# Optimization experiments

Measured on AMD Instinct MI355X. Metric: run time of the kernel, lower is better.

The kernel has to match this reference:

```python
import jax, jax.numpy as jnp
import numpy as np

G = 128          # voxel grid extent per axis
B = G + 2        # key base, allows coords in [-1, G] after +1 shift
N_PTS = 100000
C_IN = 32
C_OUT = 32


def _key(c):
    # c: [..., 3] int32 voxel coords in [-1, G]; unique linear key per voxel
    return ((c[..., 0] + 1) * B + (c[..., 1] + 1)) * B + (c[..., 2] + 1)


def setup_inputs() -> dict:
    key = jax.random.key(0)
    k1, k2, k3 = jax.random.split(key, 3)
    positions = jax.random.randint(k1, (N_PTS, 3), 0, G, dtype=jnp.int32)
    features = jax.random.normal(k2, (N_PTS, C_IN), dtype=jnp.float32)
    # per-offset filter matrices, [K^3, Cin, Cout], fan-in style init
    weight = jax.random.normal(k3, (27, C_IN, C_OUT), dtype=jnp.float32) * (1.0 / np.sqrt(27 * C_IN))
    return {"features": features, "positions": positions, "weight": weight}


def reference(features, positions, weight):
    # Submanifold sparse conv: output at the same sparse positions as input.
    # For each of the 27 kernel offsets, hash-lookup the neighbor voxel,
    # gather its feature (or 0 if absent), matmul with the per-offset filter,
    # accumulate. use_bias=False, normalize=False, voxel_size=1.0, offset=0.
    n = features.shape[0]
    keys = _key(positions)                      # [N]
    order = jnp.argsort(keys)
    sk = keys[order]                            # sorted keys (hash table)

    ax = jnp.arange(-1, 2, dtype=jnp.int32)
    off = jnp.stack(jnp.meshgrid(ax, ax, ax, indexing="ij"), axis=-1).reshape(27, 3)

    qk = _key(positions[None, :, :] + off[:, None, :])          # [27, N]
    pos_idx = jnp.clip(jnp.searchsorted(sk, qk), 0, n - 1)      # [27, N]
    match = sk[pos_idx] == qk                                   # neighbor exists?
    gidx = order[pos_idx]                                       # original index of neighbor

    gf = jnp.where(match[..., None], features[gidx], 0.0)       # [27, N, Cin] gather
    out = jnp.einsum("onc,ocd->nd", gf, weight)                 # scatter-accumulate via reduce over o
    return out
```

## Files before the change

kernel.cpp:

```cpp
#include <hip/hip_runtime.h>


#define GRID_B 130
#define GRID_CELLS 2197000
#define BM_WORDS 68704
#define C 32
#define NTHR 256
#define PTS 64
#define CAP 24

__global__ void build_grid_kernel(const int* __restrict__ pos,
                                  int* __restrict__ grid,
                                  unsigned int* __restrict__ bm, int n) {
    int i = blockIdx.x * blockDim.x + threadIdx.x;
    if (i >= n) return;
    int x = pos[3 * i + 0] + 1;
    int y = pos[3 * i + 1] + 1;
    int z = pos[3 * i + 2] + 1;
    int key = (x * GRID_B + y) * GRID_B + z;
    atomicMax(&grid[key], n - i);
    atomicOr(&bm[key >> 5], 1u << (key & 31));
}

__global__ __launch_bounds__(NTHR)
void conv_kernel(const float* __restrict__ feat,
                 const int* __restrict__ pos,
                 const float* __restrict__ w,
                 const int* __restrict__ grid,
                 const unsigned int* __restrict__ bm,
                 float* __restrict__ out, int n) {
    __shared__ int   s_cnt[27];
    __shared__ int   s_list[27][CAP];
    __shared__ int   s_rep[PTS];
    __shared__ int   s_pos[PTS * 3];
    __shared__ float s_acc[PTS][C];

    const int tid = threadIdx.x;
    const int pt_base = blockIdx.x * PTS;

    if (tid < 27) s_cnt[tid] = 0;
    for (int u = tid; u < PTS * 3; u += NTHR) {
        int g = pt_base * 3 + u;
        if (g < n * 3) s_pos[u] = pos[g];
    }
    __syncthreads();

    for (int t = tid; t < PTS * 9; t += NTHR) {
        int pl = t / 9;
        int xy = t - pl * 9;
        if (pt_base + pl < n) {
            int dx = xy / 3;
            int dy = xy - dx * 3;
            int x0 = s_pos[pl * 3 + 0] + dx;
            int y0 = s_pos[pl * 3 + 1] + dy;
            int k0 = (x0 * GRID_B + y0) * GRID_B + s_pos[pl * 3 + 2];
            unsigned int w0 = bm[(k0 >> 5)];
            unsigned int w1 = bm[(k0 >> 5) + 1];
            unsigned int bits =
                (unsigned int)((((unsigned long long)w1 << 32) | w0) >> (k0 & 31)) & 7u;
            int obase = xy * 3;
            if (xy == 4) {
                s_rep[pl] = n - grid[k0 + 1];
                bits &= 5u;
            }
            while (bits) {
                int oz = __ffs(bits) - 1;
                bits &= bits - 1;
                int v = grid[k0 + oz];
                int slot = atomicAdd(&s_cnt[obase + oz], 1);
                if (slot < CAP) s_list[obase + oz][slot] = (pl << 17) | (n - v);
            }
        }
    }
    __syncthreads();

    {
        const int cout = tid & 31;
        float wreg[32];
        #pragma unroll
        for (int c = 0; c < 32; ++c) wreg[c] = w[13 * 1024 + c * 32 + cout];
        for (int u = tid; u < PTS * C; u += NTHR) {
            int pl = u >> 5;
            if (pt_base + pl < n) {
                const float4* __restrict__ f4 = (const float4*)(feat + (size_t)s_rep[pl] * C);
                float acc = 0.0f;
                #pragma unroll
                for (int k = 0; k < 8; ++k) {
                    float4 fv = f4[k];
                    acc = fmaf(fv.x, wreg[4 * k + 0], acc);
                    acc = fmaf(fv.y, wreg[4 * k + 1], acc);
                    acc = fmaf(fv.z, wreg[4 * k + 2], acc);
                    acc = fmaf(fv.w, wreg[4 * k + 3], acc);
                }
                s_acc[pl][cout] = acc;
            }
        }
    }
    __syncthreads();

    {
        const int wv = tid >> 6;
        const int lane = tid & 63;
        const int cout = lane & 31;
        const int half = lane >> 5;
        for (int o = wv; o < 27; o += 4) {
            if (o == 13) continue;
            int cnt = min(s_cnt[o], CAP);
            if (cnt == 0) continue;
            float wreg[32];
            #pragma unroll
            for (int c = 0; c < 32; ++c) wreg[c] = w[o * 1024 + c * 32 + cout];
            for (int e = half; e < cnt; e += 2) {
                int packed = s_list[o][e];
                int pl = packed >> 17;
                int j  = packed & 0x1FFFF;
                const float4* __restrict__ f4 = (const float4*)(feat + (size_t)j * C);
                float acc = 0.0f;
                #pragma unroll
                for (int k = 0; k < 8; ++k) {
                    float4 fv = f4[k];
                    acc = fmaf(fv.x, wreg[4 * k + 0], acc);
                    acc = fmaf(fv.y, wreg[4 * k + 1], acc);
                    acc = fmaf(fv.z, wreg[4 * k + 2], acc);
                    acc = fmaf(fv.w, wreg[4 * k + 3], acc);
                }
                atomicAdd(&s_acc[pl][cout], acc);
            }
        }
    }
    __syncthreads();

    {
        const int base = pt_base * C;
        const int lim = n * C - base;
        for (int u = tid; u < PTS * C && u < lim; u += NTHR)
            out[base + u] = s_acc[u >> 5][u & 31];
    }
}

extern "C" void kernel_launch(void* const* d_in, const int* in_sizes, int n_in,
                              void* d_out, int out_size, void* d_ws, size_t ws_size,
                              hipStream_t stream) {
    const float* features = (const float*)d_in[0];
    const int*   positions = (const int*)d_in[1];
    const float* weight = (const float*)d_in[2];
    float* out = (float*)d_out;
    const int n = in_sizes[0] / C;

    int* grid = (int*)d_ws;
    unsigned int* bm = (unsigned int*)(grid + GRID_CELLS);
    hipMemsetAsync(d_ws, 0, (size_t)(GRID_CELLS + BM_WORDS) * sizeof(int), stream);

    build_grid_kernel<<<(n + 255) / 256, 256, 0, stream>>>(positions, grid, bm, n);

    conv_kernel<<<(n + PTS - 1) / PTS, NTHR, 0, stream>>>(features, positions, weight,
                                                          grid, bm, out, n);
}
```

Measured before the change: 130.3 us.

## Defer grid index lookups to a separate pass and pair neighbor gathers

Neighbor discovery now stores only the voxel key and the point index. A second parallel pass over all list slots and representatives then resolves the grid lookups, so the dependent global loads are spread evenly across threads instead of serialized inside the bitmask loop. The accumulation loop also handles two neighbor entries per iteration, issuing both feature-row loads before the FMAs to raise memory-level parallelism. The costs are an extra barrier and pass, higher register pressure from holding 16 float4 values, and a key width of 22 bits that must fit the grid size.

Result: no change. 131.1 us (+0.6%).

```diff
diff --git a/kernel.cpp b/kernel.cpp
--- a/kernel.cpp
+++ b/kernel.cpp
@@ -60,16 +60,32 @@
                 (unsigned int)((((unsigned long long)w1 << 32) | w0) >> (k0 & 31)) & 7u;
             int obase = xy * 3;
             if (xy == 4) {
-                s_rep[pl] = n - grid[k0 + 1];
+                s_rep[pl] = k0 + 1;
                 bits &= 5u;
             }
             while (bits) {
                 int oz = __ffs(bits) - 1;
                 bits &= bits - 1;
-                int v = grid[k0 + oz];
                 int slot = atomicAdd(&s_cnt[obase + oz], 1);
-                if (slot < CAP) s_list[obase + oz][slot] = (pl << 17) | (n - v);
+                if (slot < CAP) s_list[obase + oz][slot] = (pl << 22) | (k0 + oz);
             }
+        }
+    }
+    __syncthreads();
+
+    for (int t = tid; t < 27 * CAP + PTS; t += NTHR) {
+        if (t < 27 * CAP) {
+            int o = t / CAP;
+            int slot = t - o * CAP;
+            if (o != 13 && slot < min(s_cnt[o], CAP)) {
+                unsigned int e = (unsigned int)s_list[o][slot];
+                int v = grid[e & 0x3FFFFF];
+                s_list[o][slot] = (int)((e >> 22) << 17) | (n - v);
+            }
+        } else {
+            int pl = t - 27 * CAP;
+            if (pt_base + pl < n)
+                s_rep[pl] = n - grid[s_rep[pl]];
         }
     }
     __syncthreads();
@@ -110,21 +126,31 @@
             float wreg[32];
             #pragma unroll
             for (int c = 0; c < 32; ++c) wreg[c] = w[o * 1024 + c * 32 + cout];
-            for (int e = half; e < cnt; e += 2) {
-                int packed = s_list[o][e];
-                int pl = packed >> 17;
-                int j  = packed & 0x1FFFF;
-                const float4* __restrict__ f4 = (const float4*)(feat + (size_t)j * C);
-                float acc = 0.0f;
+            for (int e0 = half * 2; e0 < cnt; e0 += 4) {
+                int pk0 = s_list[o][e0];
+                int h1 = (e0 + 1 < cnt) ? 1 : 0;
+                int pk1 = s_list[o][e0 + h1];
+                const float4* __restrict__ A = (const float4*)(feat + (size_t)(pk0 & 0x1FFFF) * C);
+                const float4* __restrict__ B = (const float4*)(feat + (size_t)(pk1 & 0x1FFFF) * C);
+                float4 av[8], bv[8];
+                #pragma unroll
+                for (int k = 0; k < 8; ++k) av[k] = A[k];
+                #pragma unroll
+                for (int k = 0; k < 8; ++k) bv[k] = B[k];
+                float acca = 0.0f, accb = 0.0f;
                 #pragma unroll
                 for (int k = 0; k < 8; ++k) {
-                    float4 fv = f4[k];
-                    acc = fmaf(fv.x, wreg[4 * k + 0], acc);
-                    acc = fmaf(fv.y, wreg[4 * k + 1], acc);
-                    acc = fmaf(fv.z, wreg[4 * k + 2], acc);
-                    acc = fmaf(fv.w, wreg[4 * k + 3], acc);
+                    acca = fmaf(av[k].x, wreg[4 * k + 0], acca);
+                    acca = fmaf(av[k].y, wreg[4 * k + 1], acca);
+                    acca = fmaf(av[k].z, wreg[4 * k + 2], acca);
+                    acca = fmaf(av[k].w, wreg[4 * k + 3], acca);
+                    accb = fmaf(bv[k].x, wreg[4 * k + 0], accb);
+                    accb = fmaf(bv[k].y, wreg[4 * k + 1], accb);
+                    accb = fmaf(bv[k].z, wreg[4 * k + 2], accb);
+                    accb = fmaf(bv[k].w, wreg[4 * k + 3], accb);
                 }
-                atomicAdd(&s_acc[pl][cout], acc);
+                atomicAdd(&s_acc[pk0 >> 17][cout], acca);
+                if (h1) atomicAdd(&s_acc[pk1 >> 17][cout], accb);
             }
         }
     }
```

## Stage gathered neighbor feature rows into LDS via async global_load_lds

Applied to the files above, without the earlier changes.

Defers grid index lookups into a separate pass, builds a prefix-summed compact row index per offset, then gathers all needed feature rows (center plus neighbors) into shared memory with global_load_lds before the matmuls. Both the center and the neighbor accumulation loops now read rows from LDS instead of issuing scattered global float4 loads per output channel. Each gathered row is fetched once rather than once per lane group. This adds about 24 KB of LDS, which lowers occupancy, and adds extra barriers and a prefix-scan phase. Rows past ROWS_CAP are silently dropped, which could skip neighbors in dense blocks.

Result: no change. 128.2 us (-1.6%).

```diff
diff --git a/kernel.cpp b/kernel.cpp
--- a/kernel.cpp
+++ b/kernel.cpp
@@ -8,6 +8,7 @@
 #define NTHR 256
 #define PTS 64
 #define CAP 24
+#define ROWS_CAP 192
 
 __global__ void build_grid_kernel(const int* __restrict__ pos,
                                   int* __restrict__ grid,
@@ -30,10 +31,14 @@
                  const unsigned int* __restrict__ bm,
                  float* __restrict__ out, int n) {
     __shared__ int   s_cnt[27];
+    __shared__ int   s_seg[27];
+    __shared__ int   s_total;
     __shared__ int   s_list[27][CAP];
     __shared__ int   s_rep[PTS];
+    __shared__ int   s_jidx[ROWS_CAP];
     __shared__ int   s_pos[PTS * 3];
-    __shared__ float s_acc[PTS][C];
+    __shared__ __align__(16) float s_rows[ROWS_CAP][C];
+    __shared__ __align__(16) float s_acc[PTS][C];
 
     const int tid = threadIdx.x;
     const int pt_base = blockIdx.x * PTS;
@@ -60,40 +65,85 @@
                 (unsigned int)((((unsigned long long)w1 << 32) | w0) >> (k0 & 31)) & 7u;
             int obase = xy * 3;
             if (xy == 4) {
-                s_rep[pl] = n - grid[k0 + 1];
+                s_rep[pl] = k0 + 1;
                 bits &= 5u;
             }
             while (bits) {
                 int oz = __ffs(bits) - 1;
                 bits &= bits - 1;
-                int v = grid[k0 + oz];
                 int slot = atomicAdd(&s_cnt[obase + oz], 1);
-                if (slot < CAP) s_list[obase + oz][slot] = (pl << 17) | (n - v);
-            }
-        }
-    }
-    __syncthreads();
-
-    {
+                if (slot < CAP) s_list[obase + oz][slot] = (pl << 22) | (k0 + oz);
+            }
+        }
+    }
+    __syncthreads();
+
+    if (tid < 64) {
+        int o = tid;
+        int c = (o < 27 && o != 13) ? min(s_cnt[o], CAP) : 0;
+        int x = c;
+        #pragma unroll
+        for (int d = 1; d < 32; d <<= 1) {
+            int y = __shfl_up(x, d, 64);
+            if (tid >= d) x += y;
+        }
+        if (o < 27) s_seg[o] = PTS + x - c;
+        if (o == 26) s_total = PTS + x;
+    }
+    __syncthreads();
+
+    for (int t = tid; t < 27 * CAP + PTS; t += NTHR) {
+        if (t < 27 * CAP) {
+            int o = t / CAP;
+            int slot = t - o * CAP;
+            if (o != 13 && slot < min(s_cnt[o], CAP)) {
+                int f = s_seg[o] + slot;
+                if (f < ROWS_CAP)
+                    s_jidx[f] = n - grid[s_list[o][slot] & 0x3FFFFF];
+            }
+        } else {
+            int pl = t - 27 * CAP;
+            s_jidx[pl] = (pt_base + pl < n) ? (n - grid[s_rep[pl]]) : 0;
+        }
+    }
+    __syncthreads();
+
+    {
+        int totc = min(s_total, ROWS_CAP);
+        int lane = tid & 63, wv = tid >> 6;
+        int nI = (totc + 7) >> 3;
+        for (int i = wv; i < nI; i += 4) {
+            int f = (i << 3) + (lane >> 3);
+            int j = s_jidx[min(f, totc - 1)];
+            const float* g = feat + (size_t)j * C + ((lane & 7) << 2);
+            __builtin_amdgcn_global_load_lds(
+                (const __attribute__((address_space(1))) unsigned int*)g,
+                (__attribute__((address_space(3))) unsigned int*)(&s_rows[i << 3][0]),
+                16, 0, 0);
+        }
+    }
+    asm volatile("s_waitcnt vmcnt(0)" ::: "memory");
+    __syncthreads();
+
+    {
+        const int hw8 = tid >> 5;
         const int cout = tid & 31;
+        const int cnt13 = min(PTS, n - pt_base);
         float wreg[32];
         #pragma unroll
         for (int c = 0; c < 32; ++c) wreg[c] = w[13 * 1024 + c * 32 + cout];
-        for (int u = tid; u < PTS * C; u += NTHR) {
-            int pl = u >> 5;
-            if (pt_base + pl < n) {
-                const float4* __restrict__ f4 = (const float4*)(feat + (size_t)s_rep[pl] * C);
-                float acc = 0.0f;
-                #pragma unroll
-                for (int k = 0; k < 8; ++k) {
-                    float4 fv = f4[k];
-                    acc = fmaf(fv.x, wreg[4 * k + 0], acc);
-                    acc = fmaf(fv.y, wreg[4 * k + 1], acc);
-                    acc = fmaf(fv.z, wreg[4 * k + 2], acc);
-                    acc = fmaf(fv.w, wreg[4 * k + 3], acc);
-                }
-                s_acc[pl][cout] = acc;
-            }
+        for (int e = hw8; e < cnt13; e += 8) {
+            const float4* R = (const float4*)(&s_rows[e][0]);
+            float acc = 0.0f;
+            #pragma unroll
+            for (int k = 0; k < 8; ++k) {
+                float4 rv = R[k];
+                acc = fmaf(rv.x, wreg[4 * k + 0], acc);
+                acc = fmaf(rv.y, wreg[4 * k + 1], acc);
+                acc = fmaf(rv.z, wreg[4 * k + 2], acc);
+                acc = fmaf(rv.w, wreg[4 * k + 3], acc);
+            }
+            s_acc[e][cout] = acc;
         }
     }
     __syncthreads();
@@ -107,22 +157,23 @@
             if (o == 13) continue;
             int cnt = min(s_cnt[o], CAP);
             if (cnt == 0) continue;
+            int seg = s_seg[o];
             float wreg[32];
             #pragma unroll
             for (int c = 0; c < 32; ++c) wreg[c] = w[o * 1024 + c * 32 + cout];
             for (int e = half; e < cnt; e += 2) {
-                int packed = s_list[o][e];
-                int pl = packed >> 17;
-                int j  = packed & 0x1FFFF;
-                const float4* __restrict__ f4 = (const float4*)(feat + (size_t)j * C);
+                int f = seg + e;
+                if (f >= ROWS_CAP) break;
+                int pl = ((unsigned int)s_list[o][e]) >> 22;
+                const float4* R = (const float4*)(&s_rows[f][0]);
                 float acc = 0.0f;
                 #pragma unroll
                 for (int k = 0; k < 8; ++k) {
-                    float4 fv = f4[k];
-                    acc = fmaf(fv.x, wreg[4 * k + 0], acc);
-                    acc = fmaf(fv.y, wreg[4 * k + 1], acc);
-                    acc = fmaf(fv.z, wreg[4 * k + 2], acc);
-                    acc = fmaf(fv.w, wreg[4 * k + 3], acc);
+                    float4 rv = R[k];
+                    acc = fmaf(rv.x, wreg[4 * k + 0], acc);
+                    acc = fmaf(rv.y, wreg[4 * k + 1], acc);
+                    acc = fmaf(rv.z, wreg[4 * k + 2], acc);
+                    acc = fmaf(rv.w, wreg[4 * k + 3], acc);
                 }
                 atomicAdd(&s_acc[pl][cout], acc);
             }
```
